# Optimization experiments

Measured on AMD Instinct MI355X. Metric: run time of the kernel, lower is better.

## Reference

```python
import jax, jax.numpy as jnp
import numpy as np

EMB = 128
HEAD = 8
QKV = 16
SQRT_EMB = 11.313708498984761
CLIP = 10.0
B, P, N = 64, 100, 1000


def setup_inputs() -> dict:
    key = jax.random.key(0)
    ks = jax.random.split(key, 12)
    encoded_last_node = jax.random.normal(ks[0], (B, P, EMB), jnp.float32)
    load = jax.random.uniform(ks[1], (B, P), jnp.float32)
    time = jax.random.uniform(ks[2], (B, P), jnp.float32)
    cur_dist = jax.random.uniform(ks[3], (B, P, N), jnp.float32)
    mask_bits = jax.random.uniform(ks[4], (B, P, N)) < 0.1
    ninf_mask = jnp.where(mask_bits, -1e9, 0.0).astype(jnp.float32)
    noise = jax.random.uniform(ks[5], (B, P, N), jnp.float32)
    encoded_nodes = jax.random.normal(ks[6], (B, N, EMB), jnp.float32)
    s = 1.0 / np.sqrt(EMB)
    Wq = jax.random.uniform(ks[7], (EMB + 2, HEAD * QKV), jnp.float32, -s, s)
    Wk = jax.random.uniform(ks[8], (EMB, HEAD * QKV), jnp.float32, -s, s)
    Wv = jax.random.uniform(ks[9], (EMB, HEAD * QKV), jnp.float32, -s, s)
    Wc = jax.random.uniform(ks[10], (HEAD * QKV, EMB), jnp.float32, -s, s)
    bc = jax.random.uniform(ks[11], (EMB,), jnp.float32, -s, s)
    return {"encoded_last_node": encoded_last_node, "load": load, "time": time,
            "cur_dist": cur_dist, "ninf_mask": ninf_mask, "noise": noise,
            "encoded_nodes": encoded_nodes, "Wq": Wq, "Wk": Wk, "Wv": Wv,
            "Wc": Wc, "bc": bc}


def _heads(x):
    # (B, n, H*D) -> (B, H, n, D)
    b, n, _ = x.shape
    return x.reshape(b, n, HEAD, QKV).transpose(0, 2, 1, 3)


def reference(encoded_last_node, load, time, cur_dist, ninf_mask, noise,
              encoded_nodes, Wq, Wk, Wv, Wc, bc):
    # set_kv
    k = _heads(encoded_nodes @ Wk)   # (B,H,N,D)
    v = _heads(encoded_nodes @ Wv)   # (B,H,N,D)

    # query from last node + load + time
    input_cat = jnp.concatenate(
        [encoded_last_node, load[:, :, None], time[:, :, None]], axis=2)
    q = _heads(input_cat @ Wq)       # (B,H,P,D)

    # multi-head attention with rank3 ninf mask
    score = jnp.einsum('bhpd,bhnd->bhpn', q, k) / jnp.sqrt(
        jnp.asarray(QKV, jnp.float32))
    score = score + ninf_mask[:, None, :, :]
    weights = jax.nn.softmax(score, axis=3)
    out = jnp.einsum('bhpn,bhnd->bhpd', weights, v)
    out_concat = out.transpose(0, 2, 1, 3).reshape(B, P, HEAD * QKV)
    mh_atten_out = out_concat @ Wc + bc            # (B,P,EMB)

    # single-head pointer logits
    score2 = jnp.einsum('bpe,bne->bpn', mh_atten_out, encoded_nodes)
    score_scaled = score2 / SQRT_EMB

    # heuristic / noise blend
    st_cost = cur_dist + cur_dist
    raw_heuristic = -jnp.log(st_cost + 1e-6)
    a = 1.0 / (1.0 + 2.0 ** ((100.0 - N) / 50.0))
    b = 1.0 - a
    mixed_signal = a * raw_heuristic + b * noise
    s = score_scaled + mixed_signal
    score_clipped = CLIP * jnp.tanh(s)
    score_masked = score_clipped + ninf_mask
    probs = jax.nn.softmax(score_masked, axis=2)
    return probs
```

## Files before the change

kernel.cpp:

```cpp
#include <hip/hip_runtime.h>
#include <hip/hip_bf16.h>

#define B_   64
#define P_   100
#define N_   1000
#define EMB_ 128
#define HEAD_ 8
#define QKV_ 16
#define QT   4

constexpr double kTwoPowNeg18 = 3.814697265625e-06;
constexpr double kA_d = 1.0 / (1.0 + kTwoPowNeg18);

__global__ __launch_bounds__(256) void kv_proj(
    const float* __restrict__ en, const float* __restrict__ Wk,
    const float* __restrict__ Wv, float* __restrict__ K2, float* __restrict__ V2)
{
    __shared__ __align__(16) float e_s[32][128];
    const int t = threadIdx.x;
    const int j = t & 127;
    const int half = t >> 7;
    const int r0 = blockIdx.x * 32;

    {
        const float4* src = (const float4*)(en + (size_t)r0 * 128);
        float4* dst = (float4*)&e_s[0][0];
        #pragma unroll
        for (int k = 0; k < 4; ++k) dst[t + 256 * k] = src[t + 256 * k];
    }
    __syncthreads();

    float ak[16], av[16];
    #pragma unroll
    for (int r = 0; r < 16; ++r) { ak[r] = 0.f; av[r] = 0.f; }

    const int rb = half * 16;
    for (int i = 0; i < 128; ++i) {
        const float wk = Wk[i * 128 + j];
        const float wv = Wv[i * 128 + j];
        #pragma unroll
        for (int r = 0; r < 16; ++r) {
            const float e = e_s[rb + r][i];
            ak[r] = fmaf(e, wk, ak[r]);
            av[r] = fmaf(e, wv, av[r]);
        }
    }

    const int h = j >> 4, d = j & 15;
    #pragma unroll
    for (int r = 0; r < 16; ++r) {
        const int row = r0 + rb + r;
        const int bb = row / N_;
        const int n = row - bb * N_;
        const size_t idx = ((size_t)(bb * HEAD_ + h) * N_ + n) * 16 + d;
        K2[idx] = ak[r];
        V2[idx] = av[r];
    }
}

__global__ __launch_bounds__(128) void q_proj(
    const float* __restrict__ eln, const float* __restrict__ load_,
    const float* __restrict__ time_, const float* __restrict__ Wq,
    float* __restrict__ Q)
{
    __shared__ float e_s[8][130];
    const int j  = threadIdx.x;
    const int r0 = blockIdx.x * 8;

    #pragma unroll
    for (int r = 0; r < 8; ++r) {
        const int row = r0 + r;
        e_s[r][j] = eln[(size_t)row * 128 + j];
        if (j == 0) {
            e_s[r][128] = load_[row];
            e_s[r][129] = time_[row];
        }
    }
    __syncthreads();

    float a[8];
    #pragma unroll
    for (int r = 0; r < 8; ++r) a[r] = 0.f;

    for (int i = 0; i < 130; ++i) {
        const float w = Wq[i * 128 + j];
        #pragma unroll
        for (int r = 0; r < 8; ++r)
            a[r] = fmaf(e_s[r][i], w, a[r]);
    }

    #pragma unroll
    for (int r = 0; r < 8; ++r)
        Q[(size_t)(r0 + r) * 128 + j] = a[r];
}

__global__ __launch_bounds__(256) void attn_ptr(
    const float* __restrict__ K2, const float* __restrict__ V2,
    const float* __restrict__ Q, const float* __restrict__ en,
    const float* __restrict__ Wc, const float* __restrict__ bc,
    const float* __restrict__ cur_dist, const float* __restrict__ ninf,
    const float* __restrict__ noise, float* __restrict__ probs)
{
    __shared__ __align__(16) float sc[QT][1008];
    __shared__ __align__(16) float nf_s[QT][N_];
    __shared__ __align__(16) float q_s[QT][128];
    __shared__ __align__(16) float out_s[QT][128];
    __shared__ __align__(16) float mh_s[QT][128];
    __shared__ __align__(16) float part_s[4][QT][HEAD_][16];
    __shared__ float invden_s[HEAD_][QT];

    const int blk  = blockIdx.x;
    const int b    = blk / (P_ / QT);
    const int p0   = (blk % (P_ / QT)) * QT;
    const int bp0  = b * P_ + p0;
    const int t    = threadIdx.x;
    const int lane = t & 63;
    const int wv   = t >> 6;

    {
        const float4* qsrc = (const float4*)(Q + (size_t)bp0 * 128);
        float4* qdst = (float4*)&q_s[0][0];
        if (t < 128) qdst[t] = qsrc[t];
        const float4* nsrc = (const float4*)(ninf + (size_t)bp0 * N_);
        float4* ndst = (float4*)&nf_s[0][0];
        for (int i = t; i < N_; i += 256) ndst[i] = nsrc[i];
    }
    __syncthreads();

    for (int h = 0; h < HEAD_; ++h) {
        float qr[QT][16];
        #pragma unroll
        for (int q = 0; q < QT; ++q)
            #pragma unroll
            for (int i = 0; i < 16; ++i)
                qr[q][i] = q_s[q][h * 16 + i];

        const float* Kh = K2 + (size_t)(b * HEAD_ + h) * N_ * 16;
        for (int n = t; n < N_; n += 256) {
            const float4* kr = (const float4*)(Kh + (size_t)n * 16);
            const float4 k0 = kr[0], k1 = kr[1], k2 = kr[2], k3 = kr[3];
            #pragma unroll
            for (int q = 0; q < QT; ++q) {
                float d = k0.x * qr[q][0]  + k0.y * qr[q][1]
                        + k0.z * qr[q][2]  + k0.w * qr[q][3]
                        + k1.x * qr[q][4]  + k1.y * qr[q][5]
                        + k1.z * qr[q][6]  + k1.w * qr[q][7]
                        + k2.x * qr[q][8]  + k2.y * qr[q][9]
                        + k2.z * qr[q][10] + k2.w * qr[q][11]
                        + k3.x * qr[q][12] + k3.y * qr[q][13]
                        + k3.z * qr[q][14] + k3.w * qr[q][15];
                sc[q][n] = d * 0.25f + nf_s[q][n];
            }
        }
        __syncthreads();

        {
            const int q = wv;
            float m = -INFINITY;
            for (int n = lane; n < N_; n += 64) m = fmaxf(m, sc[q][n]);
            #pragma unroll
            for (int off = 32; off > 0; off >>= 1) m = fmaxf(m, __shfl_xor(m, off));
            float s = 0.f;
            for (int n = lane; n < N_; n += 64) {
                const float e = __expf(sc[q][n] - m);
                sc[q][n] = e;
                s += e;
            }
            #pragma unroll
            for (int off = 32; off > 0; off >>= 1) s += __shfl_xor(s, off);
            if (lane == 0) invden_s[h][q] = 1.f / s;
        }
        __syncthreads();

        {
            const int c = lane & 3, g = lane >> 2;
            const float* Vh = V2 + (size_t)(b * HEAD_ + h) * N_ * 16 + 4 * c;
            const int n0 = wv * 250;
            float4 a0 = {0.f, 0.f, 0.f, 0.f}, a1 = a0, a2 = a0, a3 = a0;
            #pragma unroll 4
            for (int i = 0; i < 16; ++i) {
                const int nn = 16 * i + g;
                if (nn < 250) {
                    const int n = n0 + nn;
                    const float4 v4 = *(const float4*)(Vh + (size_t)n * 16);
                    const float w0 = sc[0][n], w1 = sc[1][n];
                    const float w2 = sc[2][n], w3 = sc[3][n];
                    a0.x = fmaf(w0, v4.x, a0.x); a0.y = fmaf(w0, v4.y, a0.y);
                    a0.z = fmaf(w0, v4.z, a0.z); a0.w = fmaf(w0, v4.w, a0.w);
                    a1.x = fmaf(w1, v4.x, a1.x); a1.y = fmaf(w1, v4.y, a1.y);
                    a1.z = fmaf(w1, v4.z, a1.z); a1.w = fmaf(w1, v4.w, a1.w);
                    a2.x = fmaf(w2, v4.x, a2.x); a2.y = fmaf(w2, v4.y, a2.y);
                    a2.z = fmaf(w2, v4.z, a2.z); a2.w = fmaf(w2, v4.w, a2.w);
                    a3.x = fmaf(w3, v4.x, a3.x); a3.y = fmaf(w3, v4.y, a3.y);
                    a3.z = fmaf(w3, v4.z, a3.z); a3.w = fmaf(w3, v4.w, a3.w);
                }
            }
            #pragma unroll
            for (int off = 4; off <= 32; off <<= 1) {
                a0.x += __shfl_xor(a0.x, off); a0.y += __shfl_xor(a0.y, off);
                a0.z += __shfl_xor(a0.z, off); a0.w += __shfl_xor(a0.w, off);
                a1.x += __shfl_xor(a1.x, off); a1.y += __shfl_xor(a1.y, off);
                a1.z += __shfl_xor(a1.z, off); a1.w += __shfl_xor(a1.w, off);
                a2.x += __shfl_xor(a2.x, off); a2.y += __shfl_xor(a2.y, off);
                a2.z += __shfl_xor(a2.z, off); a2.w += __shfl_xor(a2.w, off);
                a3.x += __shfl_xor(a3.x, off); a3.y += __shfl_xor(a3.y, off);
                a3.z += __shfl_xor(a3.z, off); a3.w += __shfl_xor(a3.w, off);
            }
            if (g == 0) {
                *(float4*)&part_s[wv][0][h][4 * c] = a0;
                *(float4*)&part_s[wv][1][h][4 * c] = a1;
                *(float4*)&part_s[wv][2][h][4 * c] = a2;
                *(float4*)&part_s[wv][3][h][4 * c] = a3;
            }
        }
        __syncthreads();
    }

    for (int o = t; o < QT * HEAD_ * 16; o += 256) {
        const int q = o >> 7, rem = o & 127;
        const float s = (&part_s[0][q][0][0])[rem] + (&part_s[1][q][0][0])[rem]
                      + (&part_s[2][q][0][0])[rem] + (&part_s[3][q][0][0])[rem];
        out_s[q][rem] = s * invden_s[rem >> 4][q];
    }
    __syncthreads();

    {
        const int e = t & 127, qh = t >> 7;
        float a0 = bc[e], a1 = a0;
        for (int i = 0; i < 128; ++i) {
            const float w = Wc[i * 128 + e];
            a0 = fmaf(out_s[qh][i], w, a0);
            a1 = fmaf(out_s[qh + 2][i], w, a1);
        }
        mh_s[qh][e] = a0;
        mh_s[qh + 2][e] = a1;
    }
    __syncthreads();

    const float* Eb = en + (size_t)b * N_ * 128;
    for (int n = t; n < N_; n += 256) {
        const float4* er = (const float4*)(Eb + (size_t)n * 128);
        const float4* m0 = (const float4*)mh_s[0];
        const float4* m1 = (const float4*)mh_s[1];
        const float4* m2 = (const float4*)mh_s[2];
        const float4* m3 = (const float4*)mh_s[3];
        float d0 = 0.f, d1 = 0.f, d2 = 0.f, d3 = 0.f;
        #pragma unroll 8
        for (int i = 0; i < 32; ++i) {
            const float4 e4 = er[i];
            const float4 a = m0[i], b4 = m1[i], c = m2[i], dd = m3[i];
            d0 += e4.x * a.x  + e4.y * a.y  + e4.z * a.z  + e4.w * a.w;
            d1 += e4.x * b4.x + e4.y * b4.y + e4.z * b4.z + e4.w * b4.w;
            d2 += e4.x * c.x  + e4.y * c.y  + e4.z * c.z  + e4.w * c.w;
            d3 += e4.x * dd.x + e4.y * dd.y + e4.z * dd.z + e4.w * dd.w;
        }
        sc[0][n] = d0; sc[1][n] = d1; sc[2][n] = d2; sc[3][n] = d3;
    }
    __syncthreads();

    {
        const int q  = wv;
        const int bp = bp0 + q;
        const float* cd = cur_dist + (size_t)bp * N_;
        const float* nz = noise    + (size_t)bp * N_;
        const float A   = (float)kA_d;
        const float Bc2 = (float)(1.0 - kA_d);

        float m = -INFINITY;
        for (int n = lane; n < N_; n += 64) {
            const float s2 = sc[q][n] / 11.3137085f;
            const float st = cd[n] + cd[n];
            const float rh = -logf(st + 1e-6f);
            const float s  = s2 + A * rh + Bc2 * nz[n];
            const float sm = 10.f * tanhf(s) + nf_s[q][n];
            sc[q][n] = sm;
            m = fmaxf(m, sm);
        }
        #pragma unroll
        for (int off = 32; off > 0; off >>= 1) m = fmaxf(m, __shfl_xor(m, off));

        float s = 0.f;
        for (int n = lane; n < N_; n += 64) {
            const float e = __expf(sc[q][n] - m);
            sc[q][n] = e;
            s += e;
        }
        #pragma unroll
        for (int off = 32; off > 0; off >>= 1) s += __shfl_xor(s, off);

        const float inv = 1.f / s;
        float* out = probs + (size_t)bp * N_;
        for (int n = lane; n < N_; n += 64) out[n] = sc[q][n] * inv;
    }
}

extern "C" void kernel_launch(void* const* d_in, const int* in_sizes, int n_in,
                              void* d_out, int out_size, void* d_ws, size_t ws_size,
                              hipStream_t stream)
{
    const float* eln      = (const float*)d_in[0];
    const float* load_    = (const float*)d_in[1];
    const float* time_    = (const float*)d_in[2];
    const float* cur_dist = (const float*)d_in[3];
    const float* ninf     = (const float*)d_in[4];
    const float* noise    = (const float*)d_in[5];
    const float* en       = (const float*)d_in[6];
    const float* Wq       = (const float*)d_in[7];
    const float* Wk       = (const float*)d_in[8];
    const float* Wv       = (const float*)d_in[9];
    const float* Wc       = (const float*)d_in[10];
    const float* bc       = (const float*)d_in[11];
    float* probs = (float*)d_out;

    float* K2 = (float*)d_ws;
    float* V2 = K2 + (size_t)B_ * HEAD_ * N_ * 16;
    float* Q  = V2 + (size_t)B_ * HEAD_ * N_ * 16;

    kv_proj<<<(B_ * N_) / 32, 256, 0, stream>>>(en, Wk, Wv, K2, V2);
    q_proj<<<(B_ * P_) / 8, 128, 0, stream>>>(eln, load_, time_, Wq, Q);
    attn_ptr<<<(B_ * P_) / QT, 256, 0, stream>>>(K2, V2, Q, en, Wc, bc,
                                                 cur_dist, ninf, noise, probs);
}
```

Measured before the change: 554.1 us.

## Split fused attention kernel into per-head attention and pointer epilogue kernels

Splits the monolithic attention+pointer kernel into an attention kernel launched per (batch, head, query tile) that writes head outputs to a workspace, and a separate epilogue kernel that does the output projection, pointer logits and final softmax. This is meant to give eight times more blocks with much less shared memory each, raising occupancy and parallelism, at the cost of an extra launch and a global round trip for the head outputs. It also vectorises the K/V and Q projection inner loops with float4 shared-memory reads, and processes two node rows per thread in the pointer dot product. The ninf mask is now read from global memory by every head's block instead of once into shared memory.

```diff
diff --git a/kernel.cpp b/kernel.cpp
--- a/kernel.cpp
+++ b/kernel.cpp
@@ -35,14 +35,20 @@
     for (int r = 0; r < 16; ++r) { ak[r] = 0.f; av[r] = 0.f; }
 
     const int rb = half * 16;
-    for (int i = 0; i < 128; ++i) {
-        const float wk = Wk[i * 128 + j];
-        const float wv = Wv[i * 128 + j];
+    for (int i4 = 0; i4 < 32; ++i4) {
+        float wk4[4], wv4[4];
+        #pragma unroll
+        for (int c = 0; c < 4; ++c) {
+            wk4[c] = Wk[(4 * i4 + c) * 128 + j];
+            wv4[c] = Wv[(4 * i4 + c) * 128 + j];
+        }
         #pragma unroll
         for (int r = 0; r < 16; ++r) {
-            const float e = e_s[rb + r][i];
-            ak[r] = fmaf(e, wk, ak[r]);
-            av[r] = fmaf(e, wv, av[r]);
+            const float4 e4 = *(const float4*)&e_s[rb + r][4 * i4];
+            ak[r] = fmaf(e4.x, wk4[0], fmaf(e4.y, wk4[1],
+                    fmaf(e4.z, wk4[2], fmaf(e4.w, wk4[3], ak[r]))));
+            av[r] = fmaf(e4.x, wv4[0], fmaf(e4.y, wv4[1],
+                    fmaf(e4.z, wv4[2], fmaf(e4.w, wv4[3], av[r]))));
         }
     }
 
@@ -63,7 +69,7 @@
     const float* __restrict__ time_, const float* __restrict__ Wq,
     float* __restrict__ Q)
 {
-    __shared__ float e_s[8][130];
+    __shared__ __align__(16) float e_s[8][132];
     const int j  = threadIdx.x;
     const int r0 = blockIdx.x * 8;
 
@@ -82,7 +88,19 @@
     #pragma unroll
     for (int r = 0; r < 8; ++r) a[r] = 0.f;
 
-    for (int i = 0; i < 130; ++i) {
+    for (int i4 = 0; i4 < 32; ++i4) {
+        float w4[4];
+        #pragma unroll
+        for (int c = 0; c < 4; ++c) w4[c] = Wq[(4 * i4 + c) * 128 + j];
+        #pragma unroll
+        for (int r = 0; r < 8; ++r) {
+            const float4 e4 = *(const float4*)&e_s[r][4 * i4];
+            a[r] = fmaf(e4.x, w4[0], fmaf(e4.y, w4[1],
+                   fmaf(e4.z, w4[2], fmaf(e4.w, w4[3], a[r]))));
+        }
+    }
+    #pragma unroll
+    for (int i = 128; i < 130; ++i) {
         const float w = Wq[i * 128 + j];
         #pragma unroll
         for (int r = 0; r < 8; ++r)
@@ -94,49 +112,53 @@
         Q[(size_t)(r0 + r) * 128 + j] = a[r];
 }
 
-__global__ __launch_bounds__(256) void attn_ptr(
+__global__ __launch_bounds__(256) void attn_heads(
     const float* __restrict__ K2, const float* __restrict__ V2,
-    const float* __restrict__ Q, const float* __restrict__ en,
-    const float* __restrict__ Wc, const float* __restrict__ bc,
-    const float* __restrict__ cur_dist, const float* __restrict__ ninf,
-    const float* __restrict__ noise, float* __restrict__ probs)
+    const float* __restrict__ Q, const float* __restrict__ ninf,
+    float* __restrict__ out_g)
 {
     __shared__ __align__(16) float sc[QT][1008];
-    __shared__ __align__(16) float nf_s[QT][N_];
-    __shared__ __align__(16) float q_s[QT][128];
-    __shared__ __align__(16) float out_s[QT][128];
-    __shared__ __align__(16) float mh_s[QT][128];
-    __shared__ __align__(16) float part_s[4][QT][HEAD_][16];
-    __shared__ float invden_s[HEAD_][QT];
-
-    const int blk  = blockIdx.x;
-    const int b    = blk / (P_ / QT);
-    const int p0   = (blk % (P_ / QT)) * QT;
-    const int bp0  = b * P_ + p0;
+    __shared__ __align__(16) float q_s[QT][16];
+    __shared__ __align__(16) float part_s[4][QT][16];
+    __shared__ float invden_s[QT];
+
+    const int blk = blockIdx.x;
+    const int b   = blk / (HEAD_ * 25);
+    const int rem = blk - b * (HEAD_ * 25);
+    const int h   = rem / 25;
+    const int pt  = rem - h * 25;
+    const int bp0 = b * P_ + pt * QT;
     const int t    = threadIdx.x;
     const int lane = t & 63;
     const int wv   = t >> 6;
 
-    {
-        const float4* qsrc = (const float4*)(Q + (size_t)bp0 * 128);
-        float4* qdst = (float4*)&q_s[0][0];
-        if (t < 128) qdst[t] = qsrc[t];
-        const float4* nsrc = (const float4*)(ninf + (size_t)bp0 * N_);
-        float4* ndst = (float4*)&nf_s[0][0];
-        for (int i = t; i < N_; i += 256) ndst[i] = nsrc[i];
-    }
-    __syncthreads();
-
-    for (int h = 0; h < HEAD_; ++h) {
-        float qr[QT][16];
-        #pragma unroll
-        for (int q = 0; q < QT; ++q)
+    if (t < 64) q_s[t >> 4][t & 15] =
+        Q[(size_t)(bp0 + (t >> 4)) * 128 + h * 16 + (t & 15)];
+    __syncthreads();
+
+    float qr[QT][16];
+    #pragma unroll
+    for (int q = 0; q < QT; ++q)
+        #pragma unroll
+        for (int c = 0; c < 4; ++c)
+            *(float4*)&qr[q][4 * c] = *(const float4*)&q_s[q][4 * c];
+
+    const float* nf0 = ninf + (size_t)bp0 * N_;
+    float msk[QT][4];
+    #pragma unroll
+    for (int i = 0; i < 4; ++i) {
+        const int n = t + 256 * i;
+        if (n < N_) {
             #pragma unroll
-            for (int i = 0; i < 16; ++i)
-                qr[q][i] = q_s[q][h * 16 + i];
-
-        const float* Kh = K2 + (size_t)(b * HEAD_ + h) * N_ * 16;
-        for (int n = t; n < N_; n += 256) {
+            for (int q = 0; q < QT; ++q) msk[q][i] = nf0[q * N_ + n];
+        }
+    }
+
+    const float* Kh = K2 + (size_t)(b * HEAD_ + h) * N_ * 16;
+    #pragma unroll
+    for (int i = 0; i < 4; ++i) {
+        const int n = t + 256 * i;
+        if (n < N_) {
             const float4* kr = (const float4*)(Kh + (size_t)n * 16);
             const float4 k0 = kr[0], k1 = kr[1], k2 = kr[2], k3 = kr[3];
             #pragma unroll
@@ -149,79 +171,101 @@
                         + k2.z * qr[q][10] + k2.w * qr[q][11]
                         + k3.x * qr[q][12] + k3.y * qr[q][13]
                         + k3.z * qr[q][14] + k3.w * qr[q][15];
-                sc[q][n] = d * 0.25f + nf_s[q][n];
+                sc[q][n] = d * 0.25f + msk[q][i];
             }
         }
-        __syncthreads();
-
-        {
-            const int q = wv;
-            float m = -INFINITY;
-            for (int n = lane; n < N_; n += 64) m = fmaxf(m, sc[q][n]);
-            #pragma unroll
-            for (int off = 32; off > 0; off >>= 1) m = fmaxf(m, __shfl_xor(m, off));
-            float s = 0.f;
-            for (int n = lane; n < N_; n += 64) {
-                const float e = __expf(sc[q][n] - m);
-                sc[q][n] = e;
-                s += e;
+    }
+    __syncthreads();
+
+    {
+        const int q = wv;
+        float m = -INFINITY;
+        for (int n = lane; n < N_; n += 64) m = fmaxf(m, sc[q][n]);
+        #pragma unroll
+        for (int off = 32; off > 0; off >>= 1) m = fmaxf(m, __shfl_xor(m, off));
+        float s = 0.f;
+        for (int n = lane; n < N_; n += 64) {
+            const float e = __expf(sc[q][n] - m);
+            sc[q][n] = e;
+            s += e;
+        }
+        #pragma unroll
+        for (int off = 32; off > 0; off >>= 1) s += __shfl_xor(s, off);
+        if (lane == 0) invden_s[q] = 1.f / s;
+    }
+    __syncthreads();
+
+    {
+        const int c = lane & 3, g = lane >> 2;
+        const float* Vh = V2 + (size_t)(b * HEAD_ + h) * N_ * 16 + 4 * c;
+        const int n0 = wv * 250;
+        float4 a0 = {0.f, 0.f, 0.f, 0.f}, a1 = a0, a2 = a0, a3 = a0;
+        #pragma unroll 4
+        for (int i = 0; i < 16; ++i) {
+            const int nn = 16 * i + g;
+            if (nn < 250) {
+                const int n = n0 + nn;
+                const float4 v4 = *(const float4*)(Vh + (size_t)n * 16);
+                const float w0 = sc[0][n], w1 = sc[1][n];
+                const float w2 = sc[2][n], w3 = sc[3][n];
+                a0.x = fmaf(w0, v4.x, a0.x); a0.y = fmaf(w0, v4.y, a0.y);
+                a0.z = fmaf(w0, v4.z, a0.z); a0.w = fmaf(w0, v4.w, a0.w);
+                a1.x = fmaf(w1, v4.x, a1.x); a1.y = fmaf(w1, v4.y, a1.y);
+                a1.z = fmaf(w1, v4.z, a1.z); a1.w = fmaf(w1, v4.w, a1.w);
+                a2.x = fmaf(w2, v4.x, a2.x); a2.y = fmaf(w2, v4.y, a2.y);
+                a2.z = fmaf(w2, v4.z, a2.z); a2.w = fmaf(w2, v4.w, a2.w);
+                a3.x = fmaf(w3, v4.x, a3.x); a3.y = fmaf(w3, v4.y, a3.y);
+                a3.z = fmaf(w3, v4.z, a3.z); a3.w = fmaf(w3, v4.w, a3.w);
             }
-            #pragma unroll
-            for (int off = 32; off > 0; off >>= 1) s += __shfl_xor(s, off);
-            if (lane == 0) invden_s[h][q] = 1.f / s;
-        }
-        __syncthreads();
-
-        {
-            const int c = lane & 3, g = lane >> 2;
-            const float* Vh = V2 + (size_t)(b * HEAD_ + h) * N_ * 16 + 4 * c;
-            const int n0 = wv * 250;
-            float4 a0 = {0.f, 0.f, 0.f, 0.f}, a1 = a0, a2 = a0, a3 = a0;
-            #pragma unroll 4
-            for (int i = 0; i < 16; ++i) {
-                const int nn = 16 * i + g;
-                if (nn < 250) {
-                    const int n = n0 + nn;
-                    const float4 v4 = *(const float4*)(Vh + (size_t)n * 16);
-                    const float w0 = sc[0][n], w1 = sc[1][n];
-                    const float w2 = sc[2][n], w3 = sc[3][n];
-                    a0.x = fmaf(w0, v4.x, a0.x); a0.y = fmaf(w0, v4.y, a0.y);
-                    a0.z = fmaf(w0, v4.z, a0.z); a0.w = fmaf(w0, v4.w, a0.w);
-                    a1.x = fmaf(w1, v4.x, a1.x); a1.y = fmaf(w1, v4.y, a1.y);
-                    a1.z = fmaf(w1, v4.z, a1.z); a1.w = fmaf(w1, v4.w, a1.w);
-                    a2.x = fmaf(w2, v4.x, a2.x); a2.y = fmaf(w2, v4.y, a2.y);
-                    a2.z = fmaf(w2, v4.z, a2.z); a2.w = fmaf(w2, v4.w, a2.w);
-                    a3.x = fmaf(w3, v4.x, a3.x); a3.y = fmaf(w3, v4.y, a3.y);
-                    a3.z = fmaf(w3, v4.z, a3.z); a3.w = fmaf(w3, v4.w, a3.w);
-                }
-            }
-            #pragma unroll
-            for (int off = 4; off <= 32; off <<= 1) {
-                a0.x += __shfl_xor(a0.x, off); a0.y += __shfl_xor(a0.y, off);
-                a0.z += __shfl_xor(a0.z, off); a0.w += __shfl_xor(a0.w, off);
-                a1.x += __shfl_xor(a1.x, off); a1.y += __shfl_xor(a1.y, off);
-                a1.z += __shfl_xor(a1.z, off); a1.w += __shfl_xor(a1.w, off);
-                a2.x += __shfl_xor(a2.x, off); a2.y += __shfl_xor(a2.y, off);
-                a2.z += __shfl_xor(a2.z, off); a2.w += __shfl_xor(a2.w, off);
-                a3.x += __shfl_xor(a3.x, off); a3.y += __shfl_xor(a3.y, off);
-                a3.z += __shfl_xor(a3.z, off); a3.w += __shfl_xor(a3.w, off);
-            }
-            if (g == 0) {
-                *(float4*)&part_s[wv][0][h][4 * c] = a0;
-                *(float4*)&part_s[wv][1][h][4 * c] = a1;
-                *(float4*)&part_s[wv][2][h][4 * c] = a2;
-                *(float4*)&part_s[wv][3][h][4 * c] = a3;
-            }
-        }
-        __syncthreads();
-    }
-
-    for (int o = t; o < QT * HEAD_ * 16; o += 256) {
-        const int q = o >> 7, rem = o & 127;
-        const float s = (&part_s[0][q][0][0])[rem] + (&part_s[1][q][0][0])[rem]
-                      + (&part_s[2][q][0][0])[rem] + (&part_s[3][q][0][0])[rem];
-        out_s[q][rem] = s * invden_s[rem >> 4][q];
-    }
+        }
+        #pragma unroll
+        for (int off = 4; off <= 32; off <<= 1) {
+            a0.x += __shfl_xor(a0.x, off); a0.y += __shfl_xor(a0.y, off);
+            a0.z += __shfl_xor(a0.z, off); a0.w += __shfl_xor(a0.w, off);
+            a1.x += __shfl_xor(a1.x, off); a1.y += __shfl_xor(a1.y, off);
+            a1.z += __shfl_xor(a1.z, off); a1.w += __shfl_xor(a1.w, off);
+            a2.x += __shfl_xor(a2.x, off); a2.y += __shfl_xor(a2.y, off);
+            a2.z += __shfl_xor(a2.z, off); a2.w += __shfl_xor(a2.w, off);
+            a3.x += __shfl_xor(a3.x, off); a3.y += __shfl_xor(a3.y, off);
+            a3.z += __shfl_xor(a3.z, off); a3.w += __shfl_xor(a3.w, off);
+        }
+        if (g == 0) {
+            *(float4*)&part_s[wv][0][4 * c] = a0;
+            *(float4*)&part_s[wv][1][4 * c] = a1;
+            *(float4*)&part_s[wv][2][4 * c] = a2;
+            *(float4*)&part_s[wv][3][4 * c] = a3;
+        }
+    }
+    __syncthreads();
+
+    if (t < 64) {
+        const int q = t >> 4, d = t & 15;
+        const float s = part_s[0][q][d] + part_s[1][q][d]
+                      + part_s[2][q][d] + part_s[3][q][d];
+        out_g[(size_t)(bp0 + q) * 128 + h * 16 + d] = s * invden_s[q];
+    }
+}
+
+__global__ __launch_bounds__(256) void ptr_epilogue(
+    const float* __restrict__ out_g, const float* __restrict__ en,
+    const float* __restrict__ Wc, const float* __restrict__ bc,
+    const float* __restrict__ cur_dist, const float* __restrict__ ninf,
+    const float* __restrict__ noise, float* __restrict__ probs)
+{
+    __shared__ __align__(16) float sc[QT][1008];
+    __shared__ __align__(16) float out_s[QT][128];
+    __shared__ __align__(16) float mh_s[QT][128];
+
+    const int blk  = blockIdx.x;
+    const int b    = blk / 25;
+    const int pt   = blk - b * 25;
+    const int bp0  = b * P_ + pt * QT;
+    const int t    = threadIdx.x;
+    const int lane = t & 63;
+    const int wv   = t >> 6;
+
+    if (t < 128)
+        ((float4*)&out_s[0][0])[t] = ((const float4*)(out_g + (size_t)bp0 * 128))[t];
     __syncthreads();
 
     {
@@ -238,23 +282,35 @@
     __syncthreads();
 
     const float* Eb = en + (size_t)b * N_ * 128;
-    for (int n = t; n < N_; n += 256) {
-        const float4* er = (const float4*)(Eb + (size_t)n * 128);
-        const float4* m0 = (const float4*)mh_s[0];
-        const float4* m1 = (const float4*)mh_s[1];
-        const float4* m2 = (const float4*)mh_s[2];
-        const float4* m3 = (const float4*)mh_s[3];
-        float d0 = 0.f, d1 = 0.f, d2 = 0.f, d3 = 0.f;
-        #pragma unroll 8
+    const float4* m0 = (const float4*)mh_s[0];
+    const float4* m1 = (const float4*)mh_s[1];
+    const float4* m2 = (const float4*)mh_s[2];
+    const float4* m3 = (const float4*)mh_s[3];
+    #pragma unroll
+    for (int half = 0; half < 2; ++half) {
+        const int na = t + half * 512;
+        const int nb = na + 256;
+        const bool vb = (nb < N_);
+        const float4* ea = (const float4*)(Eb + (size_t)na * 128);
+        const float4* eb = (const float4*)(Eb + (size_t)(vb ? nb : na) * 128);
+        float d0a = 0.f, d1a = 0.f, d2a = 0.f, d3a = 0.f;
+        float d0b = 0.f, d1b = 0.f, d2b = 0.f, d3b = 0.f;
+        #pragma unroll 4
         for (int i = 0; i < 32; ++i) {
-            const float4 e4 = er[i];
-            const float4 a = m0[i], b4 = m1[i], c = m2[i], dd = m3[i];
-            d0 += e4.x * a.x  + e4.y * a.y  + e4.z * a.z  + e4.w * a.w;
-            d1 += e4.x * b4.x + e4.y * b4.y + e4.z * b4.z + e4.w * b4.w;
-            d2 += e4.x * c.x  + e4.y * c.y  + e4.z * c.z  + e4.w * c.w;
-            d3 += e4.x * dd.x + e4.y * dd.y + e4.z * dd.z + e4.w * dd.w;
-        }
-        sc[0][n] = d0; sc[1][n] = d1; sc[2][n] = d2; sc[3][n] = d3;
+            const float4 A4 = m0[i], B4 = m1[i], C4 = m2[i], D4 = m3[i];
+            const float4 e1 = ea[i];
+            const float4 e2 = eb[i];
+            d0a += e1.x * A4.x + e1.y * A4.y + e1.z * A4.z + e1.w * A4.w;
+            d1a += e1.x * B4.x + e1.y * B4.y + e1.z * B4.z + e1.w * B4.w;
+            d2a += e1.x * C4.x + e1.y * C4.y + e1.z * C4.z + e1.w * C4.w;
+            d3a += e1.x * D4.x + e1.y * D4.y + e1.z * D4.z + e1.w * D4.w;
+            d0b += e2.x * A4.x + e2.y * A4.y + e2.z * A4.z + e2.w * A4.w;
+            d1b += e2.x * B4.x + e2.y * B4.y + e2.z * B4.z + e2.w * B4.w;
+            d2b += e2.x * C4.x + e2.y * C4.y + e2.z * C4.z + e2.w * C4.w;
+            d3b += e2.x * D4.x + e2.y * D4.y + e2.z * D4.z + e2.w * D4.w;
+        }
+        sc[0][na] = d0a; sc[1][na] = d1a; sc[2][na] = d2a; sc[3][na] = d3a;
+        if (vb) { sc[0][nb] = d0b; sc[1][nb] = d1b; sc[2][nb] = d2b; sc[3][nb] = d3b; }
     }
     __syncthreads();
 
@@ -263,6 +319,7 @@
         const int bp = bp0 + q;
         const float* cd = cur_dist + (size_t)bp * N_;
         const float* nz = noise    + (size_t)bp * N_;
+        const float* nf = ninf     + (size_t)bp * N_;
         const float A   = (float)kA_d;
         const float Bc2 = (float)(1.0 - kA_d);
 
@@ -272,7 +329,7 @@
             const float st = cd[n] + cd[n];
             const float rh = -logf(st + 1e-6f);
             const float s  = s2 + A * rh + Bc2 * nz[n];
-            const float sm = 10.f * tanhf(s) + nf_s[q][n];
+            const float sm = 10.f * tanhf(s) + nf[n];
             sc[q][n] = sm;
             m = fmaxf(m, sm);
         }
@@ -312,12 +369,14 @@
     const float* bc       = (const float*)d_in[11];
     float* probs = (float*)d_out;
 
-    float* K2 = (float*)d_ws;
-    float* V2 = K2 + (size_t)B_ * HEAD_ * N_ * 16;
-    float* Q  = V2 + (size_t)B_ * HEAD_ * N_ * 16;
+    float* K2    = (float*)d_ws;
+    float* V2    = K2 + (size_t)B_ * HEAD_ * N_ * 16;
+    float* Q     = V2 + (size_t)B_ * HEAD_ * N_ * 16;
+    float* out_g = Q  + (size_t)B_ * P_ * 128;
 
     kv_proj<<<(B_ * N_) / 32, 256, 0, stream>>>(en, Wk, Wv, K2, V2);
     q_proj<<<(B_ * P_) / 8, 128, 0, stream>>>(eln, load_, time_, Wq, Q);
-    attn_ptr<<<(B_ * P_) / QT, 256, 0, stream>>>(K2, V2, Q, en, Wc, bc,
-                                                 cur_dist, ninf, noise, probs);
-}
+    attn_heads<<<B_ * HEAD_ * (P_ / QT), 256, 0, stream>>>(K2, V2, Q, ninf, out_g);
+    ptr_epilogue<<<(B_ * P_) / QT, 256, 0, stream>>>(out_g, en, Wc, bc,
+                                                     cur_dist, ninf, noise, probs);
+}
```

Result: no change. 549.5 us (-0.8%).
